# Optimization experiments

Hardware: AMD Instinct MI355X
Metric: run time of the kernel (lower is better)

## Reference

```python
import jax, jax.numpy as jnp
import numpy as np

ALPHA = 100.0
EPS = 1e-12  # matches torch F.normalize eps


def l2norm(v, axis):
    n = jnp.linalg.norm(v, axis=axis, keepdims=True)
    return v / jnp.maximum(n, EPS)


def setup_inputs() -> dict:
    key = jax.random.key(0)
    k1, k2 = jax.random.split(key)
    x = jax.random.normal(k1, (32, 512, 32, 32), dtype=jnp.float32)
    vocabs = jax.random.uniform(k2, (64, 512), dtype=jnp.float32)  # torch.rand init
    return {"x": x, "vocabs": vocabs}


def reference(x, vocabs):
    # x: [N, C, H, W]; vocabs: [K, C]
    N, C, H, W = x.shape
    K = vocabs.shape[0]
    x = l2norm(x, axis=1)                       # normalize descriptors over C
    xf = x.reshape(N, C, H * W)                 # [N, C, P]

    # 1x1 conv with weight = 2*alpha*vocabs, bias = -alpha*||vocabs||
    w = 2.0 * ALPHA * vocabs                    # [K, C]
    b = -ALPHA * jnp.linalg.norm(vocabs, axis=1)  # [K]
    logits = jnp.einsum('ncp,kc->nkp', xf, w) + b[None, :, None]
    a = jax.nn.softmax(logits, axis=1)          # soft assignment over K

    # Distributive rewrite of sum_p a[n,k,p]*(x[n,c,p] - vocabs[k,c])
    vlad = jnp.einsum('nkp,ncp->nkc', a, xf) - a.sum(-1)[:, :, None] * vocabs[None]
    vlad = l2norm(vlad, axis=2)                 # intra-normalization
    vlad = vlad.reshape(N, K * C)
    return l2norm(vlad, axis=1)
```

## Files before the change

kernel.cpp:

```cpp
#include <hip/hip_runtime.h>
#include <math.h>
#include <stdint.h>

#define ALPHA 100.0f
#define EPSN 1e-12f

typedef __attribute__((ext_vector_type(8))) short bf16x8;
typedef __attribute__((ext_vector_type(16))) float f32x16;
typedef __attribute__((ext_vector_type(4))) float f32x4;
typedef __attribute__((ext_vector_type(4))) unsigned int u32x4;

static __device__ __forceinline__ uint32_t f2bf(float f) {
    uint32_t u = __builtin_bit_cast(uint32_t, f);
    return (u + 0x7FFFu + ((u >> 16) & 1u)) >> 16;
}
static __device__ __forceinline__ float bfhi(uint32_t u) {
    return __builtin_bit_cast(float, u & 0xFFFF0000u);
}
static __device__ __forceinline__ uint32_t packbf(float a, float b) {
    return f2bf(a) | (f2bf(b) << 16);
}
static __device__ __forceinline__ void lds_barrier() {
    asm volatile("s_waitcnt lgkmcnt(0)\n\ts_barrier" ::: "memory");
}

__global__ __launch_bounds__(64) void prep_kernel(const float* __restrict__ v,
                                                  unsigned short* __restrict__ vh,
                                                  unsigned short* __restrict__ vl,
                                                  float* __restrict__ bias,
                                                  float* __restrict__ az) {
    int k = blockIdx.x, lane = threadIdx.x;
    az[k * 64 + lane] = 0.f;
    const float* row = v + k * 512;
    float ssq = 0.f;
#pragma unroll
    for (int i = 0; i < 8; ++i) {
        int c = lane + 64 * i;
        float f = row[c];
        ssq = fmaf(f, f, ssq);
        uint32_t hi = f2bf(f);
        uint32_t lo = f2bf(f - __builtin_bit_cast(float, hi << 16));
        vh[k * 512 + c] = (unsigned short)hi;
        vl[k * 512 + c] = (unsigned short)lo;
    }
#pragma unroll
    for (int off = 32; off > 0; off >>= 1) ssq += __shfl_xor(ssq, off, 64);
    if (lane == 0) bias[k] = -ALPHA * sqrtf(ssq);
}

__global__ __launch_bounds__(512) void assign_kernel(
    const float* __restrict__ x, const unsigned short* __restrict__ vh,
    const unsigned short* __restrict__ vl, const float* __restrict__ bias,
    unsigned short* __restrict__ aT, float* __restrict__ asum) {
    __shared__ uint32_t xsh[2][16 * 132];
    __shared__ uint32_t xsl[2][16 * 132];
    __shared__ float ssq_s[16][132];
    __shared__ float ssq_l[128];
    __shared__ float bias_l[64];
    __shared__ float xchm[4][2][32];
    __shared__ float xchs[4][2][32];

    int tid = threadIdx.x, bx = blockIdx.x;
    int n = bx >> 3, pblk = (bx & 7) << 7;
    int l = tid & 63, w = tid >> 6;
    int kh = w & 1, ps = w >> 1;
    int h = l >> 5, cl = l & 31;
    int r = tid >> 5, q = tid & 31;

    if (tid < 64) bias_l[tid] = bias[tid];

    const float* xg = x + (size_t)n * 524288 + (size_t)(2 * r) * 1024 + pblk + 4 * q;
    const unsigned short* vhg = vh + (size_t)(32 * kh + cl) * 512 + 8 * h;
    const unsigned short* vlg = vl + (size_t)(32 * kh + cl) * 512 + 8 * h;

    f32x16 accA, accB;
#pragma unroll
    for (int i = 0; i < 16; ++i) { accA[i] = 0.f; accB[i] = 0.f; }
    f32x4 ssqv;
#pragma unroll
    for (int i = 0; i < 4; ++i) ssqv[i] = 0.f;

    float4 xa[3], xb[3];
    u32x4 vfh[3][2], vfl[3][2];

#define A_LOAD(slot, cc)                                                       \
    do {                                                                       \
        xa[slot] = *(const float4*)(xg + (size_t)(cc)*32768);                  \
        xb[slot] = *(const float4*)(xg + (size_t)(cc)*32768 + 1024);           \
        vfh[slot][0] = *(const u32x4*)(vhg + (cc)*32);                         \
        vfh[slot][1] = *(const u32x4*)(vhg + (cc)*32 + 16);                    \
        vfl[slot][0] = *(const u32x4*)(vlg + (cc)*32);                         \
        vfl[slot][1] = *(const u32x4*)(vlg + (cc)*32 + 16);                    \
    } while (0)
#define A_STAGE(buf, slot)                                                     \
    do {                                                                       \
        float fa[4] = {xa[slot].x, xa[slot].y, xa[slot].z, xa[slot].w};        \
        float fb[4] = {xb[slot].x, xb[slot].y, xb[slot].z, xb[slot].w};        \
        u32x4 hp, lp;                                                          \
        _Pragma("unroll") for (int i = 0; i < 4; ++i) {                        \
            uint32_t h0 = f2bf(fa[i]);                                         \
            uint32_t l0 = f2bf(fa[i] - bfhi(h0 << 16));                        \
            uint32_t h1 = f2bf(fb[i]);                                         \
            uint32_t l1 = f2bf(fb[i] - bfhi(h1 << 16));                        \
            hp[i] = h0 | (h1 << 16);                                           \
            lp[i] = l0 | (l1 << 16);                                           \
            ssqv[i] = fmaf(fa[i], fa[i], fmaf(fb[i], fb[i], ssqv[i]));         \
        }                                                                      \
        *(u32x4*)&xsh[buf][r * 132 + 4 * q] = hp;                              \
        *(u32x4*)&xsl[buf][r * 132 + 4 * q] = lp;                              \
    } while (0)
#define A_COMPUTE(buf, slot)                                                   \
    do {                                                                       \
        _Pragma("unroll") for (int s = 0; s < 2; ++s) {                        \
            int xb_ = (8 * s + 4 * h) * 132 + 32 * ps + cl;                    \
            u32x4 bhp, blp;                                                    \
            _Pragma("unroll") for (int q2 = 0; q2 < 4; ++q2) {                 \
                bhp[q2] = xsh[buf][xb_ + q2 * 132];                            \
                blp[q2] = xsl[buf][xb_ + q2 * 132];                            \
            }                                                                  \
            bf16x8 ah = __builtin_bit_cast(bf16x8, vfh[slot][s]);              \
            bf16x8 al = __builtin_bit_cast(bf16x8, vfl[slot][s]);              \
            bf16x8 xh_ = __builtin_bit_cast(bf16x8, bhp);                      \
            bf16x8 xl_ = __builtin_bit_cast(bf16x8, blp);                      \
            f32x16& accr = s ? accB : accA;                                    \
            accr = __builtin_amdgcn_mfma_f32_32x32x16_bf16(ah, xh_, accr, 0, 0, 0);\
            accr = __builtin_amdgcn_mfma_f32_32x32x16_bf16(ah, xl_, accr, 0, 0, 0);\
            accr = __builtin_amdgcn_mfma_f32_32x32x16_bf16(al, xh_, accr, 0, 0, 0);\
        }                                                                      \
    } while (0)

    A_LOAD(0, 0);
    A_LOAD(1, 1);
    A_LOAD(2, 2);
    A_STAGE(0, 0);
    lds_barrier();
#pragma unroll
    for (int cc = 0; cc < 16; ++cc) {
        if (cc < 15) A_STAGE((cc + 1) & 1, (cc + 1) % 3);
        A_COMPUTE(cc & 1, cc % 3);
        if (cc < 13) A_LOAD(cc % 3, cc + 3);
        lds_barrier();
    }
#undef A_LOAD
#undef A_STAGE
#undef A_COMPUTE

    *(f32x4*)&ssq_s[r][4 * q] = ssqv;
    __syncthreads();
    if (tid < 128) {
        float s = 0.f;
#pragma unroll
        for (int rr = 0; rr < 16; ++rr) s += ssq_s[rr][tid];
        ssq_l[tid] = s;
    }
    __syncthreads();
    float ssq = ssq_l[32 * ps + cl];
    float sinv = 1.0f / fmaxf(sqrtf(ssq), EPSN);
    float twoAs = 2.0f * ALPHA * sinv;
    float e[16];
    float m = -INFINITY;
#pragma unroll
    for (int rr = 0; rr < 16; ++rr) {
        int k = (rr & 3) + 8 * (rr >> 2) + 4 * h + 32 * kh;
        float lv = fmaf(twoAs, accA[rr] + accB[rr], bias_l[k]);
        e[rr] = lv;
        m = fmaxf(m, lv);
    }
    m = fmaxf(m, __shfl_xor(m, 32, 64));
    if (l < 32) xchm[ps][kh][l] = m;
    __syncthreads();
    m = fmaxf(m, xchm[ps][1 - kh][cl]);
    float ssum = 0.f;
#pragma unroll
    for (int rr = 0; rr < 16; ++rr) {
        e[rr] = expf(e[rr] - m);
        ssum += e[rr];
    }
    ssum += __shfl_xor(ssum, 32, 64);
    if (l < 32) xchs[ps][kh][l] = ssum;
    __syncthreads();
    ssum += xchs[ps][1 - kh][cl];
    float rs = 1.0f / ssum;
    float a2s = rs * sinv;
    unsigned short* aTn = aT + (size_t)n * 65536 + pblk + 32 * ps + cl;
#pragma unroll
    for (int rr = 0; rr < 16; ++rr) {
        int k = (rr & 3) + 8 * (rr >> 2) + 4 * h + 32 * kh;
        aTn[(size_t)k * 1024] = (unsigned short)f2bf(e[rr] * a2s);
        float red = e[rr] * rs;
#pragma unroll
        for (int off = 1; off <= 16; off <<= 1) red += __shfl_xor(red, off, 64);
        if (cl == 0) atomicAdd(&asum[n * 64 + k], red);
    }
}

static __device__ __forceinline__ void v_load(float4& qxa, float4& qxb,
                                              u32x4& qa0, u32x4& qa1,
                                              const float* xg,
                                              const unsigned short* ag, int p0) {
    qxa = *(const float4*)(xg + p0);
    qxb = *(const float4*)(xg + p0 + 32);
    qa0 = *(const u32x4*)(ag + p0);
    qa1 = *(const u32x4*)(ag + p0 + 8);
}
static __device__ __forceinline__ void v_stage(uint32_t* xtb, uint32_t* atb,
                                               const float4 qxa, const float4 qxb,
                                               const u32x4 qa0, const u32x4 qa1,
                                               int xr, int xq, int ak, int aj) {
    int xb = xr * 34 + (xq >> 1);
    *(uint2*)&xtb[xb] = make_uint2(packbf(qxa.x, qxa.y), packbf(qxa.z, qxa.w));
    *(uint2*)&xtb[xb + 16] = make_uint2(packbf(qxb.x, qxb.y), packbf(qxb.z, qxb.w));
    int ab = ak * 34 + (aj >> 1);
    *(uint2*)&atb[ab] = make_uint2(qa0[0], qa0[1]);
    *(uint2*)&atb[ab + 2] = make_uint2(qa0[2], qa0[3]);
    *(uint2*)&atb[ab + 4] = make_uint2(qa1[0], qa1[1]);
    *(uint2*)&atb[ab + 6] = make_uint2(qa1[2], qa1[3]);
}
static __device__ __forceinline__ void v_compute(const uint32_t* xtb,
                                                 const uint32_t* atb,
                                                 f32x16& acc, int kh, int h,
                                                 int cl) {
#pragma unroll
    for (int s = 0; s < 4; ++s) {
        int va = (32 * kh + cl) * 34 + 8 * s + 4 * h;
        uint2 f0 = *(const uint2*)&atb[va];
        uint2 f1 = *(const uint2*)&atb[va + 2];
        int vb = cl * 34 + 8 * s + 4 * h;
        uint2 g0 = *(const uint2*)&xtb[vb];
        uint2 g1 = *(const uint2*)&xtb[vb + 2];
        u32x4 afp, bfp;
        afp[0] = f0.x; afp[1] = f0.y; afp[2] = f1.x; afp[3] = f1.y;
        bfp[0] = g0.x; bfp[1] = g0.y; bfp[2] = g1.x; bfp[3] = g1.y;
        acc = __builtin_amdgcn_mfma_f32_32x32x16_bf16(
            __builtin_bit_cast(bf16x8, afp), __builtin_bit_cast(bf16x8, bfp),
            acc, 0, 0, 0);
    }
}

__global__ __launch_bounds__(256) void vlad_kernel(
    const float* __restrict__ x, const unsigned short* __restrict__ aT,
    const float* __restrict__ asum, const float* __restrict__ vocabs,
    float* __restrict__ out, float* __restrict__ knorm) {
    __shared__ uint32_t xt[2][32 * 34];
    __shared__ uint32_t at[2][64 * 34];
    __shared__ float cmb[2][64][16];
    __shared__ float asum_l[64];

    int tid = threadIdx.x, bx = blockIdx.x;
    int n = bx >> 4, cb = (bx & 15) << 5;
    int l = tid & 63, w = tid >> 6;
    int kh = w & 1, ps = w >> 1;
    int h = l >> 5, cl = l & 31;

    if (tid < 64) asum_l[tid] = asum[n * 64 + tid];

    int xr = tid >> 3, xq = (tid & 7) << 2;
    int ak = tid >> 2, aj = (tid & 3) << 4;

    const float* xg = x + (size_t)n * 524288 + (size_t)(cb + xr) * 1024 + xq;
    const unsigned short* ag = aT + (size_t)n * 65536 + (size_t)ak * 1024 + aj;

    f32x16 acc;
#pragma unroll
    for (int i = 0; i < 16; ++i) acc[i] = 0.f;

    float4 qxa[2], qxb[2];
    u32x4 qa0[2], qa1[2];
    v_load(qxa[0], qxb[0], qa0[0], qa1[0], xg, ag, 0);
    v_load(qxa[1], qxb[1], qa0[1], qa1[1], xg, ag, 64);
    __syncthreads();
    v_stage(xt[0], at[0], qxa[0], qxb[0], qa0[0], qa1[0], xr, xq, ak, aj);
    lds_barrier();
#pragma unroll
    for (int cc = 0; cc < 8; ++cc) {
        v_stage(xt[1], at[1], qxa[1], qxb[1], qa0[1], qa1[1], xr, xq, ak, aj);
        if (cc < 7)
            v_load(qxa[0], qxb[0], qa0[0], qa1[0], xg, ag, (2 * cc + 2) << 6);
        if (ps == 0) v_compute(xt[0], at[0], acc, kh, h, cl);
        lds_barrier();
        if (cc < 7) {
            v_stage(xt[0], at[0], qxa[0], qxb[0], qa0[0], qa1[0], xr, xq, ak, aj);
            v_load(qxa[1], qxb[1], qa0[1], qa1[1], xg, ag, (2 * cc + 3) << 6);
        }
        if (ps == 1) v_compute(xt[1], at[1], acc, kh, h, cl);
        lds_barrier();
    }
    __syncthreads();
    if (ps == 1) {
#pragma unroll
        for (int i = 0; i < 16; ++i) cmb[kh][l][i] = acc[i];
    }
    __syncthreads();
    if (ps == 0) {
#pragma unroll
        for (int i = 0; i < 16; ++i) {
            int k = (i & 3) + 8 * (i >> 2) + 4 * h + 32 * kh;
            int c = cb + cl;
            float val = acc[i] + cmb[kh][l][i];
            val = fmaf(-asum_l[k], vocabs[k * 512 + c], val);
            out[(size_t)n * 32768 + (size_t)k * 512 + c] = val;
            float t2 = val * val;
#pragma unroll
            for (int off = 1; off <= 16; off <<= 1) t2 += __shfl_xor(t2, off, 64);
            if (cl == 0) atomicAdd(&knorm[n * 64 + k], t2);
        }
    }
}

__global__ __launch_bounds__(256) void scale_kernel(float* __restrict__ out,
                                                    const float* __restrict__ knorm) {
    int n = blockIdx.y;
    int sb = blockIdx.x;
    int tid = threadIdx.x;
    __shared__ float sc[64];
    __shared__ float tots;
    if (tid < 64) {
        float kn = knorm[n * 64 + tid];
        float nk = sqrtf(kn);
        float inv = 1.0f / fmaxf(nk, EPSN);
        sc[tid] = inv;
        float t = nk * inv;
        float t2 = t * t;
#pragma unroll
        for (int off = 32; off > 0; off >>= 1) t2 += __shfl_xor(t2, off, 64);
        if (tid == 0) tots = t2;
    }
    __syncthreads();
    float invt = 1.0f / fmaxf(sqrtf(tots), EPSN);
    float* base = out + (size_t)n * 32768 + sb * 4096;
#pragma unroll
    for (int i = 0; i < 16; ++i) {
        int idx = tid + 256 * i;
        int k = (sb * 4096 + idx) >> 9;
        base[idx] *= sc[k] * invt;
    }
}

extern "C" void kernel_launch(void* const* d_in, const int* in_sizes, int n_in,
                              void* d_out, int out_size, void* d_ws, size_t ws_size,
                              hipStream_t stream) {
    const float* x = (const float*)d_in[0];
    const float* vocabs = (const float*)d_in[1];
    float* out = (float*)d_out;
    char* ws = (char*)d_ws;
    unsigned short* vh = (unsigned short*)(ws);
    unsigned short* vl = (unsigned short*)(ws + 65536);
    float* bias  = (float*)(ws + 131072);
    float* asum  = (float*)(ws + 131328);
    float* knorm = (float*)(ws + 139520);
    unsigned short* aT = (unsigned short*)(ws + 147712);

    prep_kernel<<<64, 64, 0, stream>>>(vocabs, vh, vl, bias, asum);
    assign_kernel<<<256, 512, 0, stream>>>(x, vh, vl, bias, aT, asum);
    vlad_kernel<<<512, 256, 0, stream>>>(x, aT, asum, vocabs, out, knorm);
    scale_kernel<<<dim3(8, 32), 256, 0, stream>>>(out, knorm);
}
```

Before: 144.2 us.

## Fuse assignment and VLAD aggregation into one kernel with per-tile partials

Merges the assignment kernel and the VLAD aggregation kernel. Each block keeps its soft-assignment tile in LDS and immediately multiplies it against a re-read of its own x tile (bf16 MFMA), then writes per-pixel-tile partial sums. A new combine kernel, one block per sample, reduces the 8 partials, subtracts the asum*vocab term, computes both normalizations in LDS and writes the output. This removes the aT round trip and the separate scale pass. In exchange it adds large LDS use in the fused kernel, a 32 MB partial buffer, and a combine stage running only 32 blocks.

```diff
diff --git a/kernel.cpp b/kernel.cpp
--- a/kernel.cpp
+++ b/kernel.cpp
@@ -48,10 +48,10 @@
     if (lane == 0) bias[k] = -ALPHA * sqrtf(ssq);
 }
 
-__global__ __launch_bounds__(512) void assign_kernel(
+__global__ __launch_bounds__(512) void fused_kernel(
     const float* __restrict__ x, const unsigned short* __restrict__ vh,
     const unsigned short* __restrict__ vl, const float* __restrict__ bias,
-    unsigned short* __restrict__ aT, float* __restrict__ asum) {
+    float* __restrict__ pw, float* __restrict__ asum) {
     __shared__ uint32_t xsh[2][16 * 132];
     __shared__ uint32_t xsl[2][16 * 132];
     __shared__ float ssq_s[16][132];
@@ -59,9 +59,11 @@
     __shared__ float bias_l[64];
     __shared__ float xchm[4][2][32];
     __shared__ float xchs[4][2][32];
+    __shared__ float a2f[64 * 132];
+    __shared__ uint32_t xv[128 * 68];
 
     int tid = threadIdx.x, bx = blockIdx.x;
-    int n = bx >> 3, pblk = (bx & 7) << 7;
+    int n = bx >> 3, pt = bx & 7, pblk = pt << 7;
     int l = tid & 63, w = tid >> 6;
     int kh = w & 1, ps = w >> 1;
     int h = l >> 5, cl = l & 31;
@@ -182,141 +184,126 @@
     ssum += xchs[ps][1 - kh][cl];
     float rs = 1.0f / ssum;
     float a2s = rs * sinv;
-    unsigned short* aTn = aT + (size_t)n * 65536 + pblk + 32 * ps + cl;
 #pragma unroll
     for (int rr = 0; rr < 16; ++rr) {
         int k = (rr & 3) + 8 * (rr >> 2) + 4 * h + 32 * kh;
-        aTn[(size_t)k * 1024] = (unsigned short)f2bf(e[rr] * a2s);
+        a2f[k * 132 + 32 * ps + cl] = e[rr] * a2s;
         float red = e[rr] * rs;
 #pragma unroll
         for (int off = 1; off <= 16; off <<= 1) red += __shfl_xor(red, off, 64);
         if (cl == 0) atomicAdd(&asum[n * 64 + k], red);
     }
-}
-
-static __device__ __forceinline__ void v_load(float4& qxa, float4& qxb,
-                                              u32x4& qa0, u32x4& qa1,
-                                              const float* xg,
-                                              const unsigned short* ag, int p0) {
-    qxa = *(const float4*)(xg + p0);
-    qxb = *(const float4*)(xg + p0 + 32);
-    qa0 = *(const u32x4*)(ag + p0);
-    qa1 = *(const u32x4*)(ag + p0 + 8);
-}
-static __device__ __forceinline__ void v_stage(uint32_t* xtb, uint32_t* atb,
-                                               const float4 qxa, const float4 qxb,
-                                               const u32x4 qa0, const u32x4 qa1,
-                                               int xr, int xq, int ak, int aj) {
-    int xb = xr * 34 + (xq >> 1);
-    *(uint2*)&xtb[xb] = make_uint2(packbf(qxa.x, qxa.y), packbf(qxa.z, qxa.w));
-    *(uint2*)&xtb[xb + 16] = make_uint2(packbf(qxb.x, qxb.y), packbf(qxb.z, qxb.w));
-    int ab = ak * 34 + (aj >> 1);
-    *(uint2*)&atb[ab] = make_uint2(qa0[0], qa0[1]);
-    *(uint2*)&atb[ab + 2] = make_uint2(qa0[2], qa0[3]);
-    *(uint2*)&atb[ab + 4] = make_uint2(qa1[0], qa1[1]);
-    *(uint2*)&atb[ab + 6] = make_uint2(qa1[2], qa1[3]);
-}
-static __device__ __forceinline__ void v_compute(const uint32_t* xtb,
-                                                 const uint32_t* atb,
-                                                 f32x16& acc, int kh, int h,
-                                                 int cl) {
-#pragma unroll
-    for (int s = 0; s < 4; ++s) {
-        int va = (32 * kh + cl) * 34 + 8 * s + 4 * h;
-        uint2 f0 = *(const uint2*)&atb[va];
-        uint2 f1 = *(const uint2*)&atb[va + 2];
-        int vb = cl * 34 + 8 * s + 4 * h;
-        uint2 g0 = *(const uint2*)&xtb[vb];
-        uint2 g1 = *(const uint2*)&xtb[vb + 2];
-        u32x4 afp, bfp;
-        afp[0] = f0.x; afp[1] = f0.y; afp[2] = f1.x; afp[3] = f1.y;
-        bfp[0] = g0.x; bfp[1] = g0.y; bfp[2] = g1.x; bfp[3] = g1.y;
-        acc = __builtin_amdgcn_mfma_f32_32x32x16_bf16(
-            __builtin_bit_cast(bf16x8, afp), __builtin_bit_cast(bf16x8, bfp),
-            acc, 0, 0, 0);
-    }
-}
-
-__global__ __launch_bounds__(256) void vlad_kernel(
-    const float* __restrict__ x, const unsigned short* __restrict__ aT,
-    const float* __restrict__ asum, const float* __restrict__ vocabs,
-    float* __restrict__ out, float* __restrict__ knorm) {
-    __shared__ uint32_t xt[2][32 * 34];
-    __shared__ uint32_t at[2][64 * 34];
-    __shared__ float cmb[2][64][16];
-    __shared__ float asum_l[64];
-
-    int tid = threadIdx.x, bx = blockIdx.x;
-    int n = bx >> 4, cb = (bx & 15) << 5;
-    int l = tid & 63, w = tid >> 6;
-    int kh = w & 1, ps = w >> 1;
-    int h = l >> 5, cl = l & 31;
-
-    if (tid < 64) asum_l[tid] = asum[n * 64 + tid];
-
-    int xr = tid >> 3, xq = (tid & 7) << 2;
-    int ak = tid >> 2, aj = (tid & 3) << 4;
-
-    const float* xg = x + (size_t)n * 524288 + (size_t)(cb + xr) * 1024 + xq;
-    const unsigned short* ag = aT + (size_t)n * 65536 + (size_t)ak * 1024 + aj;
-
-    f32x16 acc;
-#pragma unroll
-    for (int i = 0; i < 16; ++i) acc[i] = 0.f;
-
-    float4 qxa[2], qxb[2];
-    u32x4 qa0[2], qa1[2];
-    v_load(qxa[0], qxb[0], qa0[0], qa1[0], xg, ag, 0);
-    v_load(qxa[1], qxb[1], qa0[1], qa1[1], xg, ag, 64);
-    __syncthreads();
-    v_stage(xt[0], at[0], qxa[0], qxb[0], qa0[0], qa1[0], xr, xq, ak, aj);
-    lds_barrier();
-#pragma unroll
-    for (int cc = 0; cc < 8; ++cc) {
-        v_stage(xt[1], at[1], qxa[1], qxb[1], qa0[1], qa1[1], xr, xq, ak, aj);
-        if (cc < 7)
-            v_load(qxa[0], qxb[0], qa0[0], qa1[0], xg, ag, (2 * cc + 2) << 6);
-        if (ps == 0) v_compute(xt[0], at[0], acc, kh, h, cl);
-        lds_barrier();
-        if (cc < 7) {
-            v_stage(xt[0], at[0], qxa[0], qxb[0], qa0[0], qa1[0], xr, xq, ak, aj);
-            v_load(qxa[1], qxb[1], qa0[1], qa1[1], xg, ag, (2 * cc + 3) << 6);
-        }
-        if (ps == 1) v_compute(xt[1], at[1], acc, kh, h, cl);
-        lds_barrier();
-    }
-    __syncthreads();
-    if (ps == 1) {
-#pragma unroll
-        for (int i = 0; i < 16; ++i) cmb[kh][l][i] = acc[i];
-    }
-    __syncthreads();
-    if (ps == 0) {
-#pragma unroll
-        for (int i = 0; i < 16; ++i) {
-            int k = (i & 3) + 8 * (i >> 2) + 4 * h + 32 * kh;
-            int c = cb + cl;
-            float val = acc[i] + cmb[kh][l][i];
-            val = fmaf(-asum_l[k], vocabs[k * 512 + c], val);
-            out[(size_t)n * 32768 + (size_t)k * 512 + c] = val;
-            float t2 = val * val;
-#pragma unroll
-            for (int off = 1; off <= 16; off <<= 1) t2 += __shfl_xor(t2, off, 64);
-            if (cl == 0) atomicAdd(&knorm[n * 64 + k], t2);
-        }
-    }
-}
-
-__global__ __launch_bounds__(256) void scale_kernel(float* __restrict__ out,
-                                                    const float* __restrict__ knorm) {
-    int n = blockIdx.y;
-    int sb = blockIdx.x;
-    int tid = threadIdx.x;
+    __syncthreads();
+
+    f32x16 va0, va1, va2, va3;
+#pragma unroll
+    for (int i = 0; i < 16; ++i) { va0[i] = 0.f; va1[i] = 0.f; va2[i] = 0.f; va3[i] = 0.f; }
+
+    int g = tid >> 2, u = tid & 3;
+#pragma unroll
+    for (int r2 = 0; r2 < 4; ++r2) {
+        __syncthreads();
+        {
+            int c = (g >> 5) * 128 + r2 * 32 + (g & 31);
+            const float* xs2 = x + (size_t)n * 524288 + (size_t)c * 1024 + pblk + 32 * u;
+            float4 f0 = *(const float4*)(xs2);
+            float4 f1 = *(const float4*)(xs2 + 4);
+            float4 f2 = *(const float4*)(xs2 + 8);
+            float4 f3 = *(const float4*)(xs2 + 12);
+            float4 f4 = *(const float4*)(xs2 + 16);
+            float4 f5 = *(const float4*)(xs2 + 20);
+            float4 f6 = *(const float4*)(xs2 + 24);
+            float4 f7 = *(const float4*)(xs2 + 28);
+            u32x4 w0, w1, w2, w3;
+            w0[0] = packbf(f0.x, f0.y); w0[1] = packbf(f0.z, f0.w);
+            w0[2] = packbf(f1.x, f1.y); w0[3] = packbf(f1.z, f1.w);
+            w1[0] = packbf(f2.x, f2.y); w1[1] = packbf(f2.z, f2.w);
+            w1[2] = packbf(f3.x, f3.y); w1[3] = packbf(f3.z, f3.w);
+            w2[0] = packbf(f4.x, f4.y); w2[1] = packbf(f4.z, f4.w);
+            w2[2] = packbf(f5.x, f5.y); w2[3] = packbf(f5.z, f5.w);
+            w3[0] = packbf(f6.x, f6.y); w3[1] = packbf(f6.z, f6.w);
+            w3[2] = packbf(f7.x, f7.y); w3[3] = packbf(f7.z, f7.w);
+            int xb0 = g * 68 + 16 * u;
+            *(u32x4*)&xv[xb0] = w0;
+            *(u32x4*)&xv[xb0 + 4] = w1;
+            *(u32x4*)&xv[xb0 + 8] = w2;
+            *(u32x4*)&xv[xb0 + 12] = w3;
+        }
+        __syncthreads();
+        f32x16& vac = (r2 == 0) ? va0 : (r2 == 1) ? va1 : (r2 == 2) ? va2 : va3;
+#pragma unroll
+        for (int mm = 0; mm < 8; ++mm) {
+            int ab = (32 * kh + cl) * 132 + 16 * mm + 8 * h;
+            u32x4 af;
+#pragma unroll
+            for (int j = 0; j < 4; ++j)
+                af[j] = packbf(a2f[ab + 2 * j], a2f[ab + 2 * j + 1]);
+            int bb = (32 * ps + cl) * 68 + 8 * mm + 4 * h;
+            u32x4 bf = *(const u32x4*)&xv[bb];
+            vac = __builtin_amdgcn_mfma_f32_32x32x16_bf16(
+                __builtin_bit_cast(bf16x8, af), __builtin_bit_cast(bf16x8, bf),
+                vac, 0, 0, 0);
+        }
+    }
+    float* pwb = pw + (((size_t)n * 8 + pt) * 64) * 512;
+#pragma unroll
+    for (int r2 = 0; r2 < 4; ++r2) {
+        f32x16& vac = (r2 == 0) ? va0 : (r2 == 1) ? va1 : (r2 == 2) ? va2 : va3;
+        int c = 128 * ps + 32 * r2 + cl;
+#pragma unroll
+        for (int rr = 0; rr < 16; ++rr) {
+            int k = (rr & 3) + 8 * (rr >> 2) + 4 * h + 32 * kh;
+            pwb[(size_t)k * 512 + c] = vac[rr];
+        }
+    }
+}
+
+__global__ __launch_bounds__(512) void combine_kernel(
+    const float* __restrict__ pw, const float* __restrict__ asum,
+    const float* __restrict__ vocabs, float* __restrict__ out) {
+    __shared__ float lv[32768];
+    __shared__ float knorm_l[64];
     __shared__ float sc[64];
     __shared__ float tots;
+
+    int n = blockIdx.x, tid = threadIdx.x;
+    int kq = tid >> 7, tc = tid & 127;
+    const float* pwn = pw + (size_t)n * 262144;
+
+#pragma unroll
+    for (int ki = 0; ki < 16; ++ki) {
+        int k = kq * 16 + ki;
+        float a = asum[n * 64 + k];
+        float4 vv = *(const float4*)(vocabs + (size_t)k * 512 + 4 * tc);
+        float4 s = make_float4(0.f, 0.f, 0.f, 0.f);
+#pragma unroll
+        for (int pt = 0; pt < 8; ++pt) {
+            float4 p4 = *(const float4*)(pwn + (size_t)pt * 32768 + (size_t)k * 512 + 4 * tc);
+            s.x += p4.x; s.y += p4.y; s.z += p4.z; s.w += p4.w;
+        }
+        s.x = fmaf(-a, vv.x, s.x);
+        s.y = fmaf(-a, vv.y, s.y);
+        s.z = fmaf(-a, vv.z, s.z);
+        s.w = fmaf(-a, vv.w, s.w);
+        *(float4*)&lv[k * 512 + 4 * tc] = s;
+    }
+    __syncthreads();
+    {
+        int k2 = tid >> 3, j = tid & 7;
+        float t2 = 0.f;
+#pragma unroll
+        for (int i = 0; i < 16; ++i) {
+            float4 v4 = *(const float4*)&lv[k2 * 512 + j * 64 + 4 * i];
+            t2 += v4.x * v4.x + v4.y * v4.y + v4.z * v4.z + v4.w * v4.w;
+        }
+        t2 += __shfl_xor(t2, 1, 64);
+        t2 += __shfl_xor(t2, 2, 64);
+        t2 += __shfl_xor(t2, 4, 64);
+        if (j == 0) knorm_l[k2] = t2;
+    }
+    __syncthreads();
     if (tid < 64) {
-        float kn = knorm[n * 64 + tid];
-        float nk = sqrtf(kn);
+        float nk = sqrtf(knorm_l[tid]);
         float inv = 1.0f / fmaxf(nk, EPSN);
         sc[tid] = inv;
         float t = nk * inv;
@@ -327,12 +314,11 @@
     }
     __syncthreads();
     float invt = 1.0f / fmaxf(sqrtf(tots), EPSN);
-    float* base = out + (size_t)n * 32768 + sb * 4096;
-#pragma unroll
-    for (int i = 0; i < 16; ++i) {
-        int idx = tid + 256 * i;
-        int k = (sb * 4096 + idx) >> 9;
-        base[idx] *= sc[k] * invt;
+    float* on = out + (size_t)n * 32768;
+#pragma unroll
+    for (int i = 0; i < 64; ++i) {
+        int idx = tid + 512 * i;
+        on[idx] = lv[idx] * sc[idx >> 9] * invt;
     }
 }
 
@@ -347,11 +333,9 @@
     unsigned short* vl = (unsigned short*)(ws + 65536);
     float* bias  = (float*)(ws + 131072);
     float* asum  = (float*)(ws + 131328);
-    float* knorm = (float*)(ws + 139520);
-    unsigned short* aT = (unsigned short*)(ws + 147712);
+    float* pw    = (float*)(ws + 147712);
 
     prep_kernel<<<64, 64, 0, stream>>>(vocabs, vh, vl, bias, asum);
-    assign_kernel<<<256, 512, 0, stream>>>(x, vh, vl, bias, aT, asum);
-    vlad_kernel<<<512, 256, 0, stream>>>(x, aT, asum, vocabs, out, knorm);
-    scale_kernel<<<dim3(8, 32), 256, 0, stream>>>(out, knorm);
-}
+    fused_kernel<<<256, 512, 0, stream>>>(x, vh, vl, bias, pw, asum);
+    combine_kernel<<<32, 512, 0, stream>>>(pw, asum, vocabs, out);
+}
```

Result: slower. 152.8 us (+6.0%).
